# Performance work log

Hardware: AMD Instinct MI355X
Metric: run time of the kernel (lower is better)

## Reference

```python
import jax, jax.numpy as jnp
import numpy as np

B, S, C = 4, 2048, 1024
H = 16
D = C // H  # head_dim = 64


def setup_inputs() -> dict:
    key = jax.random.key(0)
    ks = jax.random.split(key, 5)
    scale = 0.02
    return {
        "x": jax.random.normal(ks[0], (B, S, C), dtype=jnp.float32),
        "qkv_w": jax.random.normal(ks[1], (3 * C, C), dtype=jnp.float32) * scale,
        "qkv_b": jax.random.normal(ks[2], (3 * C,), dtype=jnp.float32) * scale,
        "proj_w": jax.random.normal(ks[3], (C, C), dtype=jnp.float32) * scale,
        "proj_b": jax.random.normal(ks[4], (C,), dtype=jnp.float32) * scale,
    }


def reference(x, qkv_w, qkv_b, proj_w, proj_b):
    b, s, c = x.shape
    qkv = x @ qkv_w.T + qkv_b            # [b,s,3c] (torch Linear: x W^T + b)
    q, k, v = jnp.split(qkv, 3, axis=2)
    # [b,s,c] -> [b,h,s,d]
    def heads(t):
        return t.reshape(b, s, H, D).transpose(0, 2, 1, 3)
    q, k, v = heads(q), heads(k), heads(v)
    scores = jnp.einsum("bhqd,bhkd->bhqk", q, k) / jnp.sqrt(jnp.float32(D))
    causal = jnp.tril(jnp.ones((s, s), dtype=bool))
    scores = jnp.where(causal[None, None], scores, -jnp.inf)
    weights = jax.nn.softmax(scores, axis=-1)
    out = jnp.einsum("bhqk,bhkd->bhqd", weights, v)
    out = out.transpose(0, 2, 1, 3).reshape(b, s, c)
    return out @ proj_w.T + proj_b
```

## Files before the change

kernel.cpp:

```cpp
#include <hip/hip_runtime.h>
#include <hip/hip_bf16.h>


typedef __attribute__((ext_vector_type(8))) short short8;
typedef __attribute__((ext_vector_type(4))) float floatx4;

__device__ __forceinline__ unsigned short f2b(float f) {
    union { float f; unsigned u; } x; x.f = f;
    unsigned r = (x.u + 0x7fffu + ((x.u >> 16) & 1u)) >> 16;
    return (unsigned short)r;
}

__device__ __forceinline__ void load16_to_lds(const unsigned short* g, unsigned short* l) {
    auto gp = (const __attribute__((address_space(1))) unsigned int*)(unsigned long long)g;
    auto lp = (__attribute__((address_space(3))) unsigned int*)(unsigned int)(unsigned long long)l;
    __builtin_amdgcn_global_load_lds(gp, lp, 16, 0, 0);
}

__global__ void __launch_bounds__(256)
convert_all(const float* __restrict__ x, const float* __restrict__ w1,
            const float* __restrict__ w2, unsigned short* __restrict__ xb,
            unsigned short* __restrict__ wb1, unsigned short* __restrict__ wb2) {
    const int N0 = 2097152, N1 = 786432;
    int i = blockIdx.x * 256 + threadIdx.x;
    const float* src; unsigned short* dst; int off;
    if (i < N0)           { src = x;  dst = xb;  off = i; }
    else if (i < N0 + N1) { src = w1; dst = wb1; off = i - N0; }
    else                  { src = w2; dst = wb2; off = i - N0 - N1; }
    float4 f = ((const float4*)src)[off];
    ushort4 u;
    u.x = f2b(f.x); u.y = f2b(f.y); u.z = f2b(f.z); u.w = f2b(f.w);
    ((ushort4*)dst)[off] = u;
}

template<int MODE>
__global__ void __launch_bounds__(256)
gemm_nt(const unsigned short* __restrict__ A, const unsigned short* __restrict__ Bw,
        const float* __restrict__ bias, int M, int N, int K,
        unsigned short* __restrict__ Qo, unsigned short* __restrict__ Ko,
        unsigned short* __restrict__ Vo, float* __restrict__ Co) {
    __shared__ unsigned short As[128][64];
    __shared__ unsigned short Bs[128][64];
    const int tid = threadIdx.x;
    const int wave = tid >> 6, lane = tid & 63;
    const int lane15 = lane & 15, quad = lane >> 4;
    const int waveM = wave >> 1, waveN = wave & 1;
    const int m0 = blockIdx.y * 128, n0 = blockIdx.x * 128;
    const int swz = (lane15 & 7);

    floatx4 acc[4][4];
#pragma unroll
    for (int i = 0; i < 4; ++i)
#pragma unroll
        for (int j = 0; j < 4; ++j) acc[i][j] = (floatx4){0.f, 0.f, 0.f, 0.f};

    for (int kt = 0; kt < K; kt += 64) {
        __syncthreads();
#pragma unroll
        for (int i = 0; i < 4; ++i) {
            int idx = tid + i * 256;
            int r = idx >> 3, c = idx & 7;
            int gc = (c ^ (r & 7)) * 8;
            load16_to_lds(&A[(size_t)(m0 + r) * K + kt + gc], &As[0][0] + idx * 8);
            load16_to_lds(&Bw[(size_t)(n0 + r) * K + kt + gc], &Bs[0][0] + idx * 8);
        }
        __asm__ volatile("s_waitcnt vmcnt(0)" ::: "memory");
        __syncthreads();
#pragma unroll
        for (int ks = 0; ks < 2; ++ks) {
            short8 af[4], bfr[4];
#pragma unroll
            for (int i = 0; i < 4; ++i)
                af[i] = *(const short8*)&As[waveM * 64 + i * 16 + lane15][((ks * 4 + quad) ^ swz) * 8];
#pragma unroll
            for (int j = 0; j < 4; ++j)
                bfr[j] = *(const short8*)&Bs[waveN * 64 + j * 16 + lane15][((ks * 4 + quad) ^ swz) * 8];
#pragma unroll
            for (int i = 0; i < 4; ++i)
#pragma unroll
                for (int j = 0; j < 4; ++j)
                    acc[i][j] = __builtin_amdgcn_mfma_f32_16x16x32_bf16(af[i], bfr[j], acc[i][j], 0, 0, 0);
        }
    }

    const float QSCALE = 0.18033688011112042f;
    if (MODE == 0) {
        const int sel = n0 >> 10;
#pragma unroll
        for (int i = 0; i < 4; ++i)
#pragma unroll
            for (int j = 0; j < 4; ++j) {
                const int n = n0 + waveN * 64 + j * 16 + lane15;
                const int c = n & 1023;
                const int h = c >> 6, d = c & 63;
                const float bia = bias[n];
                const int mbase = m0 + waveM * 64 + i * 16 + quad * 4;
                const int b = mbase >> 11, s = mbase & 2047;
                const size_t bh = (size_t)(b * 16 + h);
                if (sel == 2) {
                    ushort4 w;
                    w.x = f2b(acc[i][j][0] + bia);
                    w.y = f2b(acc[i][j][1] + bia);
                    w.z = f2b(acc[i][j][2] + bia);
                    w.w = f2b(acc[i][j][3] + bia);
                    *(ushort4*)&Vo[(bh * 64 + d) * 2048 + s] = w;
                } else {
                    unsigned short* dst = (sel == 0) ? Qo : Ko;
                    const float sc = (sel == 0) ? QSCALE : 1.0f;
#pragma unroll
                    for (int r = 0; r < 4; ++r)
                        dst[(bh * 2048 + s + r) * 64 + d] = f2b((acc[i][j][r] + bia) * sc);
                }
            }
    } else {
#pragma unroll
        for (int i = 0; i < 4; ++i)
#pragma unroll
            for (int j = 0; j < 4; ++j)
#pragma unroll
                for (int r = 0; r < 4; ++r) {
                    int m = m0 + waveM * 64 + i * 16 + quad * 4 + r;
                    int n = n0 + waveN * 64 + j * 16 + lane15;
                    Co[(size_t)m * N + n] = acc[i][j][r] + bias[n];
                }
    }
}

__global__ void __launch_bounds__(256, 2)
attn_kernel(const unsigned short* __restrict__ Q, const unsigned short* __restrict__ K,
            const unsigned short* __restrict__ V, unsigned short* __restrict__ O) {
    const int S = 2048, D = 64;
    __shared__ unsigned short Ks[2][64][64];
    __shared__ unsigned short Vt[2][64][64];
    __shared__ unsigned short Ps[4][32][72];

    const int bx = blockIdx.x;
    const int bh = blockIdx.y;
    const int tid = threadIdx.x;
    const int wave = tid >> 6, lane = tid & 63;
    const int lane15 = lane & 15, quad = lane >> 4;
    const int swz = (lane15 & 7);

    const unsigned short* Qb = Q + (size_t)bh * S * D;
    const unsigned short* Kb = K + (size_t)bh * S * D;
    const unsigned short* Vb = V + (size_t)bh * D * S;
    const int b = bh >> 4, h = bh & 15;

    auto stage = [&](int buf, int kb) {
#pragma unroll
        for (int i = 0; i < 2; ++i) {
            int idx = tid + i * 256;
            int r = idx >> 3, c = idx & 7;
            int gc = (c ^ (r & 7)) * 8;
            load16_to_lds(&Kb[(size_t)(kb + r) * D + gc], &Ks[buf][0][0] + idx * 8);
            load16_to_lds(&Vb[(size_t)r * S + kb + gc], &Vt[buf][0][0] + idx * 8);
        }
    };

    for (int qi = 0; qi < 2; ++qi) {
        const int qb = qi ? bx : 15 - bx;
        const int q0 = qb * 128;
        const int ntiles = 2 * qb + 2;

        short8 qf[2][2];
#pragma unroll
        for (int mi = 0; mi < 2; ++mi) {
            int qrow = q0 + wave * 32 + mi * 16 + lane15;
#pragma unroll
            for (int ks = 0; ks < 2; ++ks)
                qf[mi][ks] = *(const short8*)&Qb[(size_t)qrow * D + ks * 32 + quad * 8];
        }

        floatx4 o[2][4];
        float l_i[2][4];
#pragma unroll
        for (int mi = 0; mi < 2; ++mi)
#pragma unroll
            for (int r = 0; r < 4; ++r) {
                o[mi][r] = (floatx4){0.f, 0.f, 0.f, 0.f};
                l_i[mi][r] = 0.f;
            }

        __syncthreads();
        stage(0, 0);

        for (int kt = 0; kt < ntiles; ++kt) {
            const int cur = kt & 1;
            const int kb = kt * 64;
            __asm__ volatile("s_waitcnt vmcnt(0)" ::: "memory");
            __syncthreads();
            if (kt + 1 < ntiles) stage(1 - cur, kb + 64);

            floatx4 sa[2][4];
#pragma unroll
            for (int mi = 0; mi < 2; ++mi)
#pragma unroll
                for (int j = 0; j < 4; ++j) sa[mi][j] = (floatx4){0.f, 0.f, 0.f, 0.f};
#pragma unroll
            for (int j = 0; j < 4; ++j)
#pragma unroll
                for (int ks = 0; ks < 2; ++ks) {
                    short8 kf = *(const short8*)&Ks[cur][j * 16 + lane15][((ks * 4 + quad) ^ swz) * 8];
#pragma unroll
                    for (int mi = 0; mi < 2; ++mi)
                        sa[mi][j] = __builtin_amdgcn_mfma_f32_16x16x32_bf16(qf[mi][ks], kf, sa[mi][j], 0, 0, 0);
                }

            if (kb + 64 > q0) {
#pragma unroll
                for (int mi = 0; mi < 2; ++mi)
#pragma unroll
                    for (int j = 0; j < 4; ++j)
#pragma unroll
                        for (int r = 0; r < 4; ++r) {
                            int key = kb + j * 16 + lane15;
                            int qq = q0 + wave * 32 + mi * 16 + quad * 4 + r;
                            if (key > qq) sa[mi][j][r] = -1e30f;
                        }
            }

#pragma unroll
            for (int mi = 0; mi < 2; ++mi) {
#pragma unroll
                for (int j = 0; j < 4; ++j)
#pragma unroll
                    for (int r = 0; r < 4; ++r)
                        sa[mi][j][r] = __builtin_amdgcn_exp2f(sa[mi][j][r]);
#pragma unroll
                for (int r = 0; r < 4; ++r)
                    l_i[mi][r] += (sa[mi][0][r] + sa[mi][1][r]) + (sa[mi][2][r] + sa[mi][3][r]);
#pragma unroll
                for (int j = 0; j < 4; ++j)
#pragma unroll
                    for (int r = 0; r < 4; ++r)
                        Ps[wave][mi * 16 + quad * 4 + r][j * 16 + lane15] = f2b(sa[mi][j][r]);
            }
            __asm__ volatile("s_waitcnt lgkmcnt(0)" ::: "memory");

            short8 pf[2][2];
#pragma unroll
            for (int mi = 0; mi < 2; ++mi)
#pragma unroll
                for (int ks = 0; ks < 2; ++ks)
                    pf[mi][ks] = *(const short8*)&Ps[wave][mi * 16 + lane15][ks * 32 + quad * 8];

#pragma unroll
            for (int jd = 0; jd < 4; ++jd)
#pragma unroll
                for (int ks = 0; ks < 2; ++ks) {
                    short8 vf = *(const short8*)&Vt[cur][jd * 16 + lane15][((ks * 4 + quad) ^ swz) * 8];
#pragma unroll
                    for (int mi = 0; mi < 2; ++mi)
                        o[mi][jd] = __builtin_amdgcn_mfma_f32_16x16x32_bf16(pf[mi][ks], vf, o[mi][jd], 0, 0, 0);
                }
        }

#pragma unroll
        for (int mi = 0; mi < 2; ++mi)
#pragma unroll
            for (int off = 8; off >= 1; off >>= 1)
#pragma unroll
                for (int r = 0; r < 4; ++r) l_i[mi][r] += __shfl_xor(l_i[mi][r], off);

#pragma unroll
        for (int mi = 0; mi < 2; ++mi)
#pragma unroll
            for (int r = 0; r < 4; ++r) {
                int qq = q0 + wave * 32 + mi * 16 + quad * 4 + r;
                float inv = 1.0f / l_i[mi][r];
#pragma unroll
                for (int jd = 0; jd < 4; ++jd)
                    O[((size_t)(b * 2048 + qq)) * 1024 + h * 64 + jd * 16 + lane15] =
                        f2b(o[mi][jd][r] * inv);
            }
    }
}

extern "C" void kernel_launch(void* const* d_in, const int* in_sizes, int n_in,
                              void* d_out, int out_size, void* d_ws, size_t ws_size,
                              hipStream_t stream) {
    const float* x      = (const float*)d_in[0];
    const float* qkv_w  = (const float*)d_in[1];
    const float* qkv_b  = (const float*)d_in[2];
    const float* proj_w = (const float*)d_in[3];
    const float* proj_b = (const float*)d_in[4];
    float* out = (float*)d_out;

    const int B = 4, S = 2048, C = 1024, M = B * S;

    char* ws = (char*)d_ws;
    size_t off = 0;
    auto alloc = [&](size_t bytes) {
        void* p = ws + off;
        off += (bytes + 255) & ~(size_t)255;
        return p;
    };
    unsigned short* xb    = (unsigned short*)alloc((size_t)M * C * 2);
    unsigned short* wqkv  = (unsigned short*)alloc((size_t)3 * C * C * 2);
    unsigned short* wproj = (unsigned short*)alloc((size_t)C * C * 2);
    unsigned short* Qb    = (unsigned short*)alloc((size_t)M * C * 2);
    unsigned short* Kb    = (unsigned short*)alloc((size_t)M * C * 2);
    unsigned short* Vb    = (unsigned short*)alloc((size_t)M * C * 2);
    unsigned short* attn  = (unsigned short*)alloc((size_t)M * C * 2);

    {
        int total4 = (M * C + 3 * C * C + C * C) / 4;
        convert_all<<<total4 / 256, 256, 0, stream>>>(x, qkv_w, proj_w, xb, wqkv, wproj);
    }

    gemm_nt<0><<<dim3(3 * C / 128, M / 128), 256, 0, stream>>>(
        xb, wqkv, qkv_b, M, 3 * C, C, Qb, Kb, Vb, nullptr);

    attn_kernel<<<dim3(8, B * 16), 256, 0, stream>>>(Qb, Kb, Vb, attn);

    gemm_nt<1><<<dim3(C / 128, M / 128), 256, 0, stream>>>(
        attn, wproj, proj_b, M, C, C, nullptr, nullptr, nullptr, out);
}
```

Baseline: 251.1 us.

## Transpose score MFMA operands so P rows are vectorized; remap blocks per XCD

Swaps the A/B operands of the QK^T MFMA so each lane holds four consecutive keys for a single query row. The probabilities can then be packed with v_cvt_pk_bf16_f32 and written to LDS as 8-byte vectors instead of 16 scalar stores. The row-sum becomes one accumulator per mi, reduced with two cross-quad shuffles plus a final redistribution shuffle. Blocks are also remapped so each XCD handles a contiguous group of batch-heads, aiming for better L2 locality of K/V.

```diff
diff --git a/kernel.cpp b/kernel.cpp
--- a/kernel.cpp
+++ b/kernel.cpp
@@ -132,10 +132,13 @@
     const int S = 2048, D = 64;
     __shared__ unsigned short Ks[2][64][64];
     __shared__ unsigned short Vt[2][64][64];
-    __shared__ unsigned short Ps[4][32][72];
-
-    const int bx = blockIdx.x;
-    const int bh = blockIdx.y;
+    __shared__ __align__(16) unsigned short Ps[4][32][72];
+
+    const int flat = blockIdx.y * 8 + blockIdx.x;
+    const int xcd = flat & 7, slot = flat >> 3;
+    const int bh = xcd * 8 + (slot & 7);
+    const int bx = slot >> 3;
+
     const int tid = threadIdx.x;
     const int wave = tid >> 6, lane = tid & 63;
     const int lane15 = lane & 15, quad = lane >> 4;
@@ -172,14 +175,13 @@
         }
 
         floatx4 o[2][4];
-        float l_i[2][4];
-#pragma unroll
-        for (int mi = 0; mi < 2; ++mi)
-#pragma unroll
-            for (int r = 0; r < 4; ++r) {
-                o[mi][r] = (floatx4){0.f, 0.f, 0.f, 0.f};
-                l_i[mi][r] = 0.f;
-            }
+        float l_acc[2];
+#pragma unroll
+        for (int mi = 0; mi < 2; ++mi) {
+            l_acc[mi] = 0.f;
+#pragma unroll
+            for (int r = 0; r < 4; ++r) o[mi][r] = (floatx4){0.f, 0.f, 0.f, 0.f};
+        }
 
         __syncthreads();
         stage(0, 0);
@@ -203,7 +205,7 @@
                     short8 kf = *(const short8*)&Ks[cur][j * 16 + lane15][((ks * 4 + quad) ^ swz) * 8];
 #pragma unroll
                     for (int mi = 0; mi < 2; ++mi)
-                        sa[mi][j] = __builtin_amdgcn_mfma_f32_16x16x32_bf16(qf[mi][ks], kf, sa[mi][j], 0, 0, 0);
+                        sa[mi][j] = __builtin_amdgcn_mfma_f32_16x16x32_bf16(kf, qf[mi][ks], sa[mi][j], 0, 0, 0);
                 }
 
             if (kb + 64 > q0) {
@@ -213,8 +215,8 @@
                     for (int j = 0; j < 4; ++j)
 #pragma unroll
                         for (int r = 0; r < 4; ++r) {
-                            int key = kb + j * 16 + lane15;
-                            int qq = q0 + wave * 32 + mi * 16 + quad * 4 + r;
+                            int key = kb + j * 16 + quad * 4 + r;
+                            int qq = q0 + wave * 32 + mi * 16 + lane15;
                             if (key > qq) sa[mi][j][r] = -1e30f;
                         }
             }
@@ -227,13 +229,18 @@
                     for (int r = 0; r < 4; ++r)
                         sa[mi][j][r] = __builtin_amdgcn_exp2f(sa[mi][j][r]);
 #pragma unroll
-                for (int r = 0; r < 4; ++r)
-                    l_i[mi][r] += (sa[mi][0][r] + sa[mi][1][r]) + (sa[mi][2][r] + sa[mi][3][r]);
-#pragma unroll
                 for (int j = 0; j < 4; ++j)
-#pragma unroll
-                    for (int r = 0; r < 4; ++r)
-                        Ps[wave][mi * 16 + quad * 4 + r][j * 16 + lane15] = f2b(sa[mi][j][r]);
+                    l_acc[mi] += (sa[mi][j][0] + sa[mi][j][1]) + (sa[mi][j][2] + sa[mi][j][3]);
+#pragma unroll
+                for (int j = 0; j < 4; ++j) {
+                    unsigned w0, w1;
+                    __asm__("v_cvt_pk_bf16_f32 %0, %1, %2"
+                            : "=v"(w0) : "v"(sa[mi][j][0]), "v"(sa[mi][j][1]));
+                    __asm__("v_cvt_pk_bf16_f32 %0, %1, %2"
+                            : "=v"(w1) : "v"(sa[mi][j][2]), "v"(sa[mi][j][3]));
+                    uint2 w; w.x = w0; w.y = w1;
+                    *(uint2*)&Ps[wave][mi * 16 + lane15][j * 16 + quad * 4] = w;
+                }
             }
             __asm__ volatile("s_waitcnt lgkmcnt(0)" ::: "memory");
 
@@ -256,18 +263,18 @@
         }
 
 #pragma unroll
-        for (int mi = 0; mi < 2; ++mi)
-#pragma unroll
-            for (int off = 8; off >= 1; off >>= 1)
-#pragma unroll
-                for (int r = 0; r < 4; ++r) l_i[mi][r] += __shfl_xor(l_i[mi][r], off);
+        for (int mi = 0; mi < 2; ++mi) {
+            l_acc[mi] += __shfl_xor(l_acc[mi], 16);
+            l_acc[mi] += __shfl_xor(l_acc[mi], 32);
+        }
 
 #pragma unroll
         for (int mi = 0; mi < 2; ++mi)
 #pragma unroll
             for (int r = 0; r < 4; ++r) {
                 int qq = q0 + wave * 32 + mi * 16 + quad * 4 + r;
-                float inv = 1.0f / l_i[mi][r];
+                float lq = __shfl(l_acc[mi], (lane & 48) + quad * 4 + r);
+                float inv = 1.0f / lq;
 #pragma unroll
                 for (int jd = 0; jd < 4; ++jd)
                     O[((size_t)(b * 2048 + qq)) * 1024 + h * 64 + jd * 16 + lane15] =
```

Result: faster. 233.4 us (-7.1%).
